# Performance work log

Measured on AMD Instinct MI355X. Metric: run time of the kernel, lower is better.

The kernel has to match this reference:

```python
import jax, jax.numpy as jnp
import numpy as np

B0, PER, T, V, E = 8, 2, 128, 50257, 4
N = B0 * PER


def setup_inputs() -> dict:
    key = jax.random.key(0)
    k1, k2, k3, k4 = jax.random.split(key, 4)
    return {
        "gen_ori_img_preds": jax.random.normal(k1, (B0, T, V), dtype=jnp.float32),
        "gen_cap_preds": jax.random.normal(k2, (N, T, V), dtype=jnp.float32),
        "masked_item_lens": jnp.full((B0,), PER, dtype=jnp.int32),
        "entities_ids": jax.random.randint(k3, (N, E), 0, V, dtype=jnp.int32),
        "prefixes_lens": jax.random.randint(k4, (N,), 1, T, dtype=jnp.int32),  # unused by forward
        "prompt_length": 20,  # unused by forward
    }


def reference(gen_ori_img_preds, gen_cap_preds, masked_item_lens, entities_ids, prefixes_lens, prompt_length):
    # gen_ori_img_preds: [B0, T, V]; gen_cap_preds: [N, T, V]; entities_ids: [N, E]
    B0_, T_, _ = gen_ori_img_preds.shape
    N_ = gen_cap_preds.shape[0]
    # repeat_interleave(arange(B0), masked_item_lens) -> map each expanded row to its source sample
    repeated = jnp.repeat(jnp.arange(B0_), masked_item_lens, total_repeat_length=N_)  # [N]
    # log_softmax gathered at entity columns: log_softmax(x)[..., e] = x[..., e] - logsumexp(x)
    lse_ori = jax.nn.logsumexp(gen_ori_img_preds, axis=-1)  # [B0, T]
    lse_gen = jax.nn.logsumexp(gen_cap_preds, axis=-1)      # [N, T]
    t_idx = jnp.arange(T_)[None, :, None]
    # gather raw logits at entity ids, broadcast over T -> [N, T, E]
    g_ori = gen_ori_img_preds[repeated[:, None, None], t_idx, entities_ids[:, None, :]] \
            - lse_ori[repeated][:, :, None]
    g_gen = jnp.take_along_axis(gen_cap_preds, entities_ids[:, None, :], axis=2) \
            - lse_gen[:, :, None]
    # mean over T per entity, difference, then mean over entities (sum / len(entity_ids_i))
    per_entity = g_ori.mean(axis=1) - g_gen.mean(axis=1)  # [N, E]
    sample_loss = per_entity.mean(axis=-1)                 # [N]
    return (-sample_loss).mean()
```

## Files before the change

### kernel.cpp

```cpp
#include <hip/hip_runtime.h>

#define B0 8
#define T  128
#define V  50257
#define E  4
#define NN 16

__global__ __launch_bounds__(256) void lse_kernel(
    const float* __restrict__ ori, const float* __restrict__ cap,
    float* __restrict__ lse) {
  const int row = blockIdx.x;
  const float* base;
  long long s;
  if (row < B0 * T) {
    base = ori;
    s = (long long)row * V;
  } else {
    base = cap;
    s = (long long)(row - B0 * T) * V;
  }
  const long long end = s + V;
  const long long s_al = (s + 3) & ~3LL;
  const int tid = threadIdx.x;

  float a0 = 0.f, a1 = 0.f, a2 = 0.f, a3 = 0.f;

  const int head = (int)(s_al - s);
  if (tid < head) a0 += __expf(base[s + tid]);

  const long long n4 = (end - s_al) >> 2;
  const float4* b4 = (const float4*)(base + s_al);
  for (long long j = tid; j < n4; j += 256) {
    const float4 v = b4[j];
    a0 += __expf(v.x);
    a1 += __expf(v.y);
    a2 += __expf(v.z);
    a3 += __expf(v.w);
  }

  const long long tstart = s_al + (n4 << 2);
  const int tail = (int)(end - tstart);
  if (tid < tail) a1 += __expf(base[tstart + tid]);

  float acc = (a0 + a1) + (a2 + a3);

  __shared__ float red[256];
  red[tid] = acc;
  __syncthreads();
  for (int w = 128; w > 0; w >>= 1) {
    if (tid < w) red[tid] += red[tid + w];
    __syncthreads();
  }
  if (tid == 0) lse[row] = __logf(red[0]);
}

__global__ __launch_bounds__(256) void finish_kernel(
    const float* __restrict__ ori, const float* __restrict__ cap,
    const int* __restrict__ mlens, const int* __restrict__ eids,
    const float* __restrict__ lse, float* __restrict__ out) {
  __shared__ int rep[NN];
  const int tid = threadIdx.x;
  if (tid == 0) {
    int idx = 0;
    for (int b = 0; b < B0 && idx < NN; ++b) {
      const int c = mlens[b];
      for (int k = 0; k < c && idx < NN; ++k) rep[idx++] = b;
    }
    const int lastv = (idx > 0) ? rep[idx - 1] : 0;
    for (; idx < NN; ++idx) rep[idx] = lastv;
  }
  __syncthreads();

  const float* lse_ori = lse;
  const float* lse_gen = lse + B0 * T;

  float sg = 0.f;
  for (int i = tid; i < NN * E * T; i += 256) {
    const int n = i / (E * T);
    const int r = i - n * (E * T);
    const int e = r / T;
    const int t = r - e * T;
    const int col = eids[n * E + e];
    sg += ori[((long long)rep[n] * T + t) * V + col]
        - cap[((long long)n * T + t) * V + col];
  }

  float sl = 0.f;
  for (int i = tid; i < NN * T; i += 256) {
    const int n = i / T;
    const int t = i - n * T;
    sl += lse_gen[n * T + t] - lse_ori[rep[n] * T + t];
  }

  __shared__ float r1[256];
  __shared__ float r2[256];
  r1[tid] = sg;
  r2[tid] = sl;
  __syncthreads();
  for (int w = 128; w > 0; w >>= 1) {
    if (tid < w) {
      r1[tid] += r1[tid + w];
      r2[tid] += r2[tid + w];
    }
    __syncthreads();
  }
  if (tid == 0) {
    out[0] = -(r1[0] / (float)(NN * E * T) + r2[0] / (float)(NN * T));
  }
}

extern "C" void kernel_launch(void* const* d_in, const int* in_sizes, int n_in,
                              void* d_out, int out_size, void* d_ws, size_t ws_size,
                              hipStream_t stream) {
  const float* ori   = (const float*)d_in[0];
  const float* cap   = (const float*)d_in[1];
  const int*   mlens = (const int*)d_in[2];
  const int*   eids  = (const int*)d_in[3];
  float* out = (float*)d_out;
  float* lse = (float*)d_ws;

  const int rows = B0 * T + NN * T;
  lse_kernel<<<rows, 256, 0, stream>>>(ori, cap, lse);
  finish_kernel<<<1, 256, 0, stream>>>(ori, cap, mlens, eids, lse, out);
}
```

Baseline: 695.4 us.

## Fuse entity gather and loss weighting into per-row LSE kernel

Each row block now gathers its own entity logits, weights its LSE by how many expanded samples map to it, and writes a per-row partial loss. A tiny reduce kernel sums the partials. This removes the serial single-block finish kernel, which did 8192 scattered gathers. The block reduction also moves from a shared-memory tree to wavefront shuffles. The cost is some redundant mlens parsing in every ori block.

```diff
diff --git a/kernel.cpp b/kernel.cpp
--- a/kernel.cpp
+++ b/kernel.cpp
@@ -5,23 +5,39 @@
 #define V  50257
 #define E  4
 #define NN 16
+#define ROWS (B0 * T + NN * T)
 
-__global__ __launch_bounds__(256) void lse_kernel(
+__global__ __launch_bounds__(256) void fused_lse_gather(
     const float* __restrict__ ori, const float* __restrict__ cap,
-    float* __restrict__ lse) {
+    const int* __restrict__ mlens, const int* __restrict__ eids,
+    float* __restrict__ partial) {
   const int row = blockIdx.x;
-  const float* base;
-  long long s;
-  if (row < B0 * T) {
-    base = ori;
-    s = (long long)row * V;
-  } else {
-    base = cap;
-    s = (long long)(row - B0 * T) * V;
+  const int tid = threadIdx.x;
+
+  __shared__ int rep_sh[NN];
+  __shared__ int cnt_sh[B0];
+  __shared__ float wsum[4];
+
+  const bool is_ori = row < B0 * T;
+  const float* base = is_ori ? ori : cap;
+  const int local = is_ori ? row : row - B0 * T;
+  const int rn = local / T;
+  const long long s = (long long)local * V;
+  const long long end = s + V;
+
+  if (is_ori && tid == 0) {
+    for (int b = 0; b < B0; ++b) cnt_sh[b] = 0;
+    int idx = 0;
+    for (int b = 0; b < B0 && idx < NN; ++b) {
+      const int c = mlens[b];
+      for (int k = 0; k < c && idx < NN; ++k) rep_sh[idx++] = b;
+    }
+    const int lastv = (idx > 0) ? rep_sh[idx - 1] : 0;
+    for (; idx < NN; ++idx) rep_sh[idx] = lastv;
+    for (int n = 0; n < NN; ++n) cnt_sh[rep_sh[n]]++;
   }
-  const long long end = s + V;
+
   const long long s_al = (s + 3) & ~3LL;
-  const int tid = threadIdx.x;
 
   float a0 = 0.f, a1 = 0.f, a2 = 0.f, a3 = 0.f;
 
@@ -44,69 +60,49 @@
 
   float acc = (a0 + a1) + (a2 + a3);
 
+  for (int o = 32; o > 0; o >>= 1) acc += __shfl_down(acc, o, 64);
+  if ((tid & 63) == 0) wsum[tid >> 6] = acc;
+  __syncthreads();
+
+  float gv = 0.f;
+  if (tid < 64) {
+    if (is_ori) {
+      const int n = tid >> 2;
+      if (rep_sh[n] == rn) gv = base[s + eids[tid]];
+    } else if (tid < E) {
+      gv = base[s + eids[rn * E + tid]];
+    }
+    for (int o = 32; o > 0; o >>= 1) gv += __shfl_down(gv, o, 64);
+  }
+
+  if (tid == 0) {
+    const float total = (wsum[0] + wsum[1]) + (wsum[2] + wsum[3]);
+    const float lse = __logf(total);
+    const float inv_nt = 1.f / (float)(NN * T);
+    const float inv_net = 1.f / (float)(NN * E * T);
+    float p;
+    if (is_ori) {
+      p = (float)cnt_sh[rn] * inv_nt * lse - gv * inv_net;
+    } else {
+      p = gv * inv_net - lse * inv_nt;
+    }
+    partial[row] = p;
+  }
+}
+
+__global__ __launch_bounds__(256) void reduce_kernel(
+    const float* __restrict__ partial, float* __restrict__ out) {
+  const int tid = threadIdx.x;
+  float a = 0.f;
+  for (int i = tid; i < ROWS; i += 256) a += partial[i];
   __shared__ float red[256];
-  red[tid] = acc;
+  red[tid] = a;
   __syncthreads();
   for (int w = 128; w > 0; w >>= 1) {
     if (tid < w) red[tid] += red[tid + w];
     __syncthreads();
   }
-  if (tid == 0) lse[row] = __logf(red[0]);
-}
-
-__global__ __launch_bounds__(256) void finish_kernel(
-    const float* __restrict__ ori, const float* __restrict__ cap,
-    const int* __restrict__ mlens, const int* __restrict__ eids,
-    const float* __restrict__ lse, float* __restrict__ out) {
-  __shared__ int rep[NN];
-  const int tid = threadIdx.x;
-  if (tid == 0) {
-    int idx = 0;
-    for (int b = 0; b < B0 && idx < NN; ++b) {
-      const int c = mlens[b];
-      for (int k = 0; k < c && idx < NN; ++k) rep[idx++] = b;
-    }
-    const int lastv = (idx > 0) ? rep[idx - 1] : 0;
-    for (; idx < NN; ++idx) rep[idx] = lastv;
-  }
-  __syncthreads();
-
-  const float* lse_ori = lse;
-  const float* lse_gen = lse + B0 * T;
-
-  float sg = 0.f;
-  for (int i = tid; i < NN * E * T; i += 256) {
-    const int n = i / (E * T);
-    const int r = i - n * (E * T);
-    const int e = r / T;
-    const int t = r - e * T;
-    const int col = eids[n * E + e];
-    sg += ori[((long long)rep[n] * T + t) * V + col]
-        - cap[((long long)n * T + t) * V + col];
-  }
-
-  float sl = 0.f;
-  for (int i = tid; i < NN * T; i += 256) {
-    const int n = i / T;
-    const int t = i - n * T;
-    sl += lse_gen[n * T + t] - lse_ori[rep[n] * T + t];
-  }
-
-  __shared__ float r1[256];
-  __shared__ float r2[256];
-  r1[tid] = sg;
-  r2[tid] = sl;
-  __syncthreads();
-  for (int w = 128; w > 0; w >>= 1) {
-    if (tid < w) {
-      r1[tid] += r1[tid + w];
-      r2[tid] += r2[tid + w];
-    }
-    __syncthreads();
-  }
-  if (tid == 0) {
-    out[0] = -(r1[0] / (float)(NN * E * T) + r2[0] / (float)(NN * T));
-  }
+  if (tid == 0) out[0] = red[0];
 }
 
 extern "C" void kernel_launch(void* const* d_in, const int* in_sizes, int n_in,
@@ -117,9 +113,8 @@
   const int*   mlens = (const int*)d_in[2];
   const int*   eids  = (const int*)d_in[3];
   float* out = (float*)d_out;
-  float* lse = (float*)d_ws;
+  float* partial = (float*)d_ws;
 
-  const int rows = B0 * T + NN * T;
-  lse_kernel<<<rows, 256, 0, stream>>>(ori, cap, lse);
-  finish_kernel<<<1, 256, 0, stream>>>(ori, cap, mlens, eids, lse, out);
+  fused_lse_gather<<<ROWS, 256, 0, stream>>>(ori, cap, mlens, eids, partial);
+  reduce_kernel<<<1, 256, 0, stream>>>(partial, out);
 }
```

After: 651.8 us. -6.3%, faster.
